# Performance work log

Hardware: AMD Instinct MI355X
Metric: run time of the kernel (lower is better)

## Reference

```python
import jax, jax.numpy as jnp
import numpy as np

B, S, F = 4, 2048, 8
D, H, L, FF = 256, 8, 2, 1024
DH = D // H
NSK, NPAT = 2000, 64
DQ = D // 4  # pattern/feat sub-embedding width


def setup_inputs() -> dict:
    key = jax.random.key(0)
    ks = jax.random.split(key, 32)
    r = lambda i, shape: jax.random.normal(ks[i], shape, jnp.float32) * 0.02
    return {
        'interactions': jax.random.randint(ks[0], (B, S), 0, 2 * NSK),
        'patterns': jax.random.randint(ks[1], (B, S), 0, NPAT),
        'forget_features': jax.random.normal(ks[2], (B, S, F), jnp.float32),
        'inter_emb': r(3, (2 * NSK, D)),
        'pattern_emb': r(4, (NPAT, DQ)),
        'feat_W': r(5, (F, DQ)), 'feat_b': jnp.zeros((DQ,), jnp.float32),
        'in_W': r(6, (D + 2 * DQ, D)), 'in_b': jnp.zeros((D,), jnp.float32),
        'time_W': r(7, (1, D)), 'time_b': jnp.zeros((D,), jnp.float32),
        'pos_W': r(8, (1, D)), 'pos_b': jnp.zeros((D,), jnp.float32),
        'Wq': r(9, (L, D, H, DH)), 'bq': jnp.zeros((L, H, DH), jnp.float32),
        'Wk': r(10, (L, D, H, DH)), 'bk': jnp.zeros((L, H, DH), jnp.float32),
        'Wv': r(11, (L, D, H, DH)), 'bv': jnp.zeros((L, H, DH), jnp.float32),
        'Wo': r(12, (L, H, DH, D)), 'bo': jnp.zeros((L, D), jnp.float32),
        'kerple_p': jnp.full((L, H, 1, 1), 0.5, jnp.float32),
        'kerple_a': jnp.zeros((L, H, 1, 1), jnp.float32),
        'ln1_g': jnp.ones((L, D), jnp.float32), 'ln1_b': jnp.zeros((L, D), jnp.float32),
        'ln2_g': jnp.ones((L, D), jnp.float32), 'ln2_b': jnp.zeros((L, D), jnp.float32),
        'ffn_W1': r(13, (L, D, FF)), 'ffn_b1': jnp.zeros((L, FF), jnp.float32),
        'ffn_W2': r(14, (L, FF, D)), 'ffn_b2': jnp.zeros((L, D), jnp.float32),
        'out_W': r(15, (D, NSK)), 'out_b': jnp.zeros((NSK,), jnp.float32),
    }


def _ln(x, g, b, eps=1e-6):
    m = jnp.mean(x, -1, keepdims=True)
    v = jnp.mean(jnp.square(x - m), -1, keepdims=True)
    return g * (x - m) * jax.lax.rsqrt(v + eps) + b


def reference(interactions, patterns, forget_features, inter_emb, pattern_emb,
              feat_W, feat_b, in_W, in_b, time_W, time_b, pos_W, pos_b,
              Wq, bq, Wk, bk, Wv, bv, Wo, bo, kerple_p, kerple_a,
              ln1_g, ln1_b, ln2_g, ln2_b, ffn_W1, ffn_b1, ffn_W2, ffn_b2,
              out_W, out_b):
    inter_e = inter_emb[interactions]                      # [B,S,D]
    pat_e = pattern_emb[patterns]                          # [B,S,D/4]
    feat_e = forget_features @ feat_W + feat_b             # [B,S,D/4]
    x = jnp.concatenate([inter_e, pat_e, feat_e], -1) @ in_W + in_b  # [B,S,D]
    elapsed = forget_features[:, :, 0:1]
    time_enc = jnp.tanh(elapsed @ time_W + time_b)
    pos = jnp.arange(S, dtype=jnp.float32)[None, :, None] / jnp.float32(S)
    pos_enc = pos @ pos_W + pos_b
    x = x + time_enc + pos_enc

    positions = jnp.arange(S, dtype=jnp.float32)
    dist = jnp.maximum(positions[:, None] - positions[None, :], 0.0)  # [S,S]
    causal_bias = jnp.triu(jnp.full((S, S), -1e9, jnp.float32), 1)    # [S,S]
    inv_sqrt_dh = 1.0 / jnp.sqrt(jnp.float32(DH))

    for i in range(L):
        p = jax.nn.softplus(kerple_p[i])                   # [H,1,1]
        a = jax.nn.softplus(kerple_a[i])
        bias = causal_bias[None] - p * jnp.log1p(a * dist[None])  # [H,S,S]
        q = jnp.einsum('bsd,dhk->bshk', x, Wq[i]) + bq[i]
        k = jnp.einsum('bsd,dhk->bshk', x, Wk[i]) + bk[i]
        v = jnp.einsum('bsd,dhk->bshk', x, Wv[i]) + bv[i]
        scores = jnp.einsum('bshk,bthk->bhst', q, k) * inv_sqrt_dh + bias[None]
        attn = jax.nn.softmax(scores, axis=-1)
        o = jnp.einsum('bhst,bthk->bshk', attn, v)
        attn_out = jnp.einsum('bshk,hkd->bsd', o, Wo[i]) + bo[i]
        x = _ln(x + attn_out, ln1_g[i], ln1_b[i])
        h = jax.nn.gelu(x @ ffn_W1[i] + ffn_b1[i], approximate=False)
        ffn_out = h @ ffn_W2[i] + ffn_b2[i]
        x = _ln(x + ffn_out, ln2_g[i], ln2_b[i])
    return x @ out_W + out_b
```

## Files before the change

kernel.cpp:

```cpp
#include <hip/hip_runtime.h>
#include <math.h>

#define SEQ   2048
#define BATCH 4
#define NTOK  8192
#define DM    256
#define NHD   8
#define DHD   32
#define DFF   1024
#define NSKC  2000

typedef __attribute__((ext_vector_type(8))) short short8;
typedef __attribute__((ext_vector_type(4))) float f32x4;
typedef unsigned short ushort_t;

#define QPRE ((float)(0.17677669529663687 * 1.4426950408889634))

#define SPERM(i) (((i) & ~31) | (((i) & 15) << 1) | (((i) >> 4) & 1))

__device__ __forceinline__ ushort_t f2bf(float x) {
    union { float f; unsigned u; } c; c.f = x;
    unsigned r = c.u + 0x7FFFu + ((c.u >> 16) & 1u);
    return (ushort_t)(r >> 16);
}

#if __has_builtin(__builtin_amdgcn_cvt_pk_bf16_f32)
typedef __attribute__((ext_vector_type(2))) __bf16 bf16x2_t;
__device__ __forceinline__ unsigned pack_bf16(float a, float b) {
    bf16x2_t r = __builtin_amdgcn_cvt_pk_bf16_f32(a, b);
    union { bf16x2_t v; unsigned u; } c; c.v = r;
    return c.u;
}
#else
__device__ __forceinline__ unsigned pack_bf16(float a, float b) {
    return (unsigned)f2bf(a) | ((unsigned)f2bf(b) << 16);
}
#endif

__device__ __forceinline__ float bf2f(ushort_t x) {
    union { unsigned u; float f; } c; c.u = ((unsigned)x) << 16;
    return c.f;
}

struct ConvSeg { const float* src; ushort_t* dst; int K; int N; int ntx; int base; int kperm; };
struct ConvArgs { ConvSeg s[14]; };

__global__ __launch_bounds__(256) void convert_kernel(ConvArgs args) {
    int bid = blockIdx.x;
    int si = 0;
#pragma unroll
    for (int i = 1; i < 14; i++) if (bid >= args.s[i].base) si = i;
    ConvSeg sg = args.s[si];
    int local = bid - sg.base;
    int ty = local / sg.ntx;
    int tx = local - ty * sg.ntx;
    int n0 = tx * 32, k0 = ty * 32;
    __shared__ float T[32][33];
    int tid = threadIdx.x;
    int tn = tid & 31, tk4 = tid >> 5;
#pragma unroll
    for (int i = 0; i < 4; i++) {
        int kl = tk4 + i * 8;
        float v = 0.0f;
        if (n0 + tn < sg.N) v = sg.src[(size_t)(k0 + kl) * sg.N + n0 + tn];
        T[kl][tn] = v;
    }
    __syncthreads();
    int tk = tid & 31, tn4 = tid >> 5;
    int tks = sg.kperm ? (((tk & 15) << 1) | ((tk >> 4) & 1)) : tk;
#pragma unroll
    for (int i = 0; i < 4; i++) {
        int nl = tn4 + i * 8;
        sg.dst[(size_t)(n0 + nl) * sg.K + k0 + tks] = f2bf(T[tk][nl]);
    }
}

__global__ __launch_bounds__(384) void concat_kernel(
    const int* __restrict__ interactions, const int* __restrict__ patterns,
    const float* __restrict__ ff, const float* __restrict__ inter_emb,
    const float* __restrict__ pattern_emb, const float* __restrict__ feat_W,
    const float* __restrict__ feat_b, ushort_t* __restrict__ out)
{
    int tok = blockIdx.x;
    int j = threadIdx.x;
    float v;
    if (j < 256) {
        v = inter_emb[(size_t)interactions[tok] * 256 + j];
    } else if (j < 320) {
        v = pattern_emb[patterns[tok] * 64 + (j - 256)];
    } else {
        int c = j - 320;
        float acc = feat_b[c];
#pragma unroll
        for (int f = 0; f < 8; f++) acc += ff[tok * 8 + f] * feat_W[f * 64 + c];
        v = acc;
    }
    out[(size_t)tok * 384 + j] = f2bf(v);
}

__global__ __launch_bounds__(256) void ln_kernel(
    float* __restrict__ x, const ushort_t* __restrict__ r,
    const float* __restrict__ g, const float* __restrict__ b,
    ushort_t* __restrict__ xb)
{
    int tok = blockIdx.x;
    int d = threadIdx.x;
    int ds = SPERM(d);
    size_t row = (size_t)tok * DM;
    float v = x[row + d] + bf2f(r[row + ds]);
    float s1 = v, s2 = v * v;
#pragma unroll
    for (int off = 32; off > 0; off >>= 1) {
        s1 += __shfl_down(s1, off, 64);
        s2 += __shfl_down(s2, off, 64);
    }
    __shared__ float red1[4], red2[4];
    int wid = d >> 6, lane = d & 63;
    if (lane == 0) { red1[wid] = s1; red2[wid] = s2; }
    __syncthreads();
    s1 = red1[0] + red1[1] + red1[2] + red1[3];
    s2 = red2[0] + red2[1] + red2[2] + red2[3];
    float mean = s1 * (1.0f / 256.0f);
    float var = s2 * (1.0f / 256.0f) - mean * mean;
    float inv = rsqrtf(var + 1e-6f);
    float nv = g[d] * (v - mean) * inv + b[d];
    x[row + d] = nv;
    xb[row + ds] = f2bf(nv);
}

__global__ __launch_bounds__(256) void gemm64(
    const ushort_t* __restrict__ A, const ushort_t* __restrict__ Bt,
    int M, int N, int K, int mode,
    float* __restrict__ Cf, ushort_t* __restrict__ Cb,
    const float* __restrict__ b0,
    const float* __restrict__ ffg, const float* __restrict__ tW,
    const float* __restrict__ tb, const float* __restrict__ pW,
    const float* __restrict__ pb)
{
    __shared__ ushort_t As[2][64][40];
    __shared__ ushort_t Bs[2][64][40];
    int m0 = blockIdx.x * 64, n0 = blockIdx.y * 64;
    int tid = threadIdx.x;
    int wv = tid >> 6, lane = tid & 63;
    int quad = lane >> 4, l16 = lane & 15;
    int srow = tid >> 2, sc = (tid & 3) << 3;

    f32x4 acc[4];
#pragma unroll
    for (int j = 0; j < 4; j++) acc[j] = (f32x4){0.f, 0.f, 0.f, 0.f};

    uint4 pa = *(const uint4*)&A[(size_t)(m0 + srow) * K + sc];
    uint4 pbv = *(const uint4*)&Bt[(size_t)(n0 + srow) * K + sc];
    *(uint4*)&As[0][srow][sc] = pa;
    *(uint4*)&Bs[0][srow][sc] = pbv;

    int mrow = wv * 16;
    for (int k0 = 0; k0 < K; k0 += 32) {
        int cur = (k0 >> 5) & 1;
        __syncthreads();
        bool more = (k0 + 32 < K);
        if (more) {
            pa = *(const uint4*)&A[(size_t)(m0 + srow) * K + k0 + 32 + sc];
            pbv = *(const uint4*)&Bt[(size_t)(n0 + srow) * K + k0 + 32 + sc];
        }
        short8 af = *(const short8*)&As[cur][mrow + l16][quad * 8];
        short8 bf0 = *(const short8*)&Bs[cur][l16][quad * 8];
        short8 bf1 = *(const short8*)&Bs[cur][16 + l16][quad * 8];
        short8 bf2 = *(const short8*)&Bs[cur][32 + l16][quad * 8];
        short8 bf3 = *(const short8*)&Bs[cur][48 + l16][quad * 8];
        acc[0] = __builtin_amdgcn_mfma_f32_16x16x32_bf16(af, bf0, acc[0], 0, 0, 0);
        acc[1] = __builtin_amdgcn_mfma_f32_16x16x32_bf16(af, bf1, acc[1], 0, 0, 0);
        acc[2] = __builtin_amdgcn_mfma_f32_16x16x32_bf16(af, bf2, acc[2], 0, 0, 0);
        acc[3] = __builtin_amdgcn_mfma_f32_16x16x32_bf16(af, bf3, acc[3], 0, 0, 0);
        if (more) {
            *(uint4*)&As[cur ^ 1][srow][sc] = pa;
            *(uint4*)&Bs[cur ^ 1][srow][sc] = pbv;
        }
    }

#pragma unroll
    for (int r = 0; r < 4; r++) {
        int m = m0 + mrow + quad * 4 + r;
        if (mode == 4) {
            int s = m & (SEQ - 1);
            float el = ffg[m * 8];
            float pos = (float)s * (1.0f / (float)SEQ);
#pragma unroll
            for (int nt = 0; nt < 4; nt += 2) {
                int nlo = n0 + nt * 16 + l16;
                int nhi = nlo + 16;
                float v0 = acc[nt][r] + b0[nlo] + tanhf(el * tW[nlo] + tb[nlo]) + pos * pW[nlo] + pb[nlo];
                float v1 = acc[nt + 1][r] + b0[nhi] + tanhf(el * tW[nhi] + tb[nhi]) + pos * pW[nhi] + pb[nhi];
                Cf[(size_t)m * N + nlo] = v0;
                Cf[(size_t)m * N + nhi] = v1;
                *(unsigned*)&Cb[(size_t)m * N + n0 + nt * 16 + 2 * l16] = pack_bf16(v0, v1);
            }
        } else {
#pragma unroll
            for (int nt = 0; nt < 4; nt += 2) {
                int nlo = n0 + nt * 16 + l16;
                float v0 = acc[nt][r] + b0[nlo];
                float v1 = acc[nt + 1][r] + b0[nlo + 16];
                *(unsigned*)&Cb[(size_t)m * N + n0 + nt * 16 + 2 * l16] = pack_bf16(v0, v1);
            }
        }
    }
}

__global__ __launch_bounds__(256) void gemm_db(
    const ushort_t* __restrict__ A, const ushort_t* __restrict__ Bt,
    int M, int N, int K, int mode,
    ushort_t* __restrict__ Cb, ushort_t* __restrict__ Ck, ushort_t* __restrict__ Cv,
    const float* __restrict__ b0, const float* __restrict__ b1,
    const float* __restrict__ b2)
{
    __shared__ ushort_t As[2][128][40];
    __shared__ ushort_t Bs[2][64][40];
    int m0 = blockIdx.x * 128, n0 = blockIdx.y * 64;
    int tid = threadIdx.x;
    int wv = tid >> 6, lane = tid & 63;
    int quad = lane >> 4, l16 = lane & 15;
    int srow = tid >> 2, sc = (tid & 3) << 3;

    f32x4 acc[2][4];
#pragma unroll
    for (int i = 0; i < 2; i++)
#pragma unroll
        for (int j = 0; j < 4; j++) acc[i][j] = (f32x4){0.f, 0.f, 0.f, 0.f};

    uint4 pa0 = *(const uint4*)&A[(size_t)(m0 + srow) * K + sc];
    uint4 pa1 = *(const uint4*)&A[(size_t)(m0 + 64 + srow) * K + sc];
    uint4 pbb = *(const uint4*)&Bt[(size_t)(n0 + srow) * K + sc];
    *(uint4*)&As[0][srow][sc] = pa0;
    *(uint4*)&As[0][64 + srow][sc] = pa1;
    *(uint4*)&Bs[0][srow][sc] = pbb;

    int msub = wv * 32;
    for (int k0 = 0; k0 < K; k0 += 32) {
        int cur = (k0 >> 5) & 1;
        __syncthreads();
        bool more = (k0 + 32 < K);
        if (more) {
            pa0 = *(const uint4*)&A[(size_t)(m0 + srow) * K + k0 + 32 + sc];
            pa1 = *(const uint4*)&A[(size_t)(m0 + 64 + srow) * K + k0 + 32 + sc];
            pbb = *(const uint4*)&Bt[(size_t)(n0 + srow) * K + k0 + 32 + sc];
        }
        short8 af0 = *(const short8*)&As[cur][msub + l16][quad * 8];
        short8 af1 = *(const short8*)&As[cur][msub + 16 + l16][quad * 8];
        short8 bf0 = *(const short8*)&Bs[cur][l16][quad * 8];
        short8 bf1 = *(const short8*)&Bs[cur][16 + l16][quad * 8];
        short8 bf2 = *(const short8*)&Bs[cur][32 + l16][quad * 8];
        short8 bf3 = *(const short8*)&Bs[cur][48 + l16][quad * 8];
        acc[0][0] = __builtin_amdgcn_mfma_f32_16x16x32_bf16(af0, bf0, acc[0][0], 0, 0, 0);
        acc[0][1] = __builtin_amdgcn_mfma_f32_16x16x32_bf16(af0, bf1, acc[0][1], 0, 0, 0);
        acc[0][2] = __builtin_amdgcn_mfma_f32_16x16x32_bf16(af0, bf2, acc[0][2], 0, 0, 0);
        acc[0][3] = __builtin_amdgcn_mfma_f32_16x16x32_bf16(af0, bf3, acc[0][3], 0, 0, 0);
        acc[1][0] = __builtin_amdgcn_mfma_f32_16x16x32_bf16(af1, bf0, acc[1][0], 0, 0, 0);
        acc[1][1] = __builtin_amdgcn_mfma_f32_16x16x32_bf16(af1, bf1, acc[1][1], 0, 0, 0);
        acc[1][2] = __builtin_amdgcn_mfma_f32_16x16x32_bf16(af1, bf2, acc[1][2], 0, 0, 0);
        acc[1][3] = __builtin_amdgcn_mfma_f32_16x16x32_bf16(af1, bf3, acc[1][3], 0, 0, 0);
        if (more) {
            *(uint4*)&As[cur ^ 1][srow][sc] = pa0;
            *(uint4*)&As[cur ^ 1][64 + srow][sc] = pa1;
            *(uint4*)&Bs[cur ^ 1][srow][sc] = pbb;
        }
    }

#pragma unroll
    for (int mt = 0; mt < 2; mt++) {
#pragma unroll
        for (int nt = 0; nt < 4; nt += 2) {
            int nlo = n0 + nt * 16 + l16;
#pragma unroll
            for (int r = 0; r < 4; r++) {
                int m = m0 + msub + mt * 16 + quad * 4 + r;
                float vlo = acc[mt][nt][r];
                float vhi = acc[mt][nt + 1][r];
                if (mode == 1) {
                    float t0 = vlo + b0[nlo];
                    float t1 = vhi + b0[nlo + 16];
                    t0 = 0.5f * t0 * (1.0f + erff(t0 * 0.70710678118654752f));
                    t1 = 0.5f * t1 * (1.0f + erff(t1 * 0.70710678118654752f));
                    *(unsigned*)&Cb[(size_t)m * N + n0 + nt * 16 + 2 * l16] = pack_bf16(t0, t1);
                } else {
                    int which = nlo >> 8, idx = nlo & 255;
                    int hh = idx >> 5;
                    int s = m & (SEQ - 1), b = m >> 11;
                    if (which == 0) {
                        float q0 = (vlo + b0[idx]) * QPRE;
                        float q1 = (vhi + b0[idx + 16]) * QPRE;
                        *(unsigned*)&Cb[(((size_t)(b * NHD + hh)) * SEQ + s) * DHD + 2 * l16] = pack_bf16(q0, q1);
                    } else if (which == 1) {
                        float k0v = vlo + b1[idx];
                        float k1v = vhi + b1[idx + 16];
                        *(unsigned*)&Ck[(((size_t)(b * NHD + hh)) * SEQ + s) * DHD + 2 * l16] = pack_bf16(k0v, k1v);
                    } else {
                        int sp = (s & ~31) | (((s & 15) << 1) | ((s >> 4) & 1));
                        Cv[(((size_t)(b * NHD + hh)) * DHD + l16) * SEQ + sp] = f2bf(vlo + b2[idx]);
                        Cv[(((size_t)(b * NHD + hh)) * DHD + l16 + 16) * SEQ + sp] = f2bf(vhi + b2[idx + 16]);
                    }
                }
            }
        }
    }
}

__global__ __launch_bounds__(256) void gemm_out(
    const ushort_t* __restrict__ A, const ushort_t* __restrict__ Bt,
    int M, int N, int K,
    float* __restrict__ Cf, const float* __restrict__ b0, int Nreal)
{
    __shared__ ushort_t As[2][128][40];
    __shared__ ushort_t Bs[2][128][40];
    int m0 = blockIdx.x * 128, n0 = blockIdx.y * 128;
    int tid = threadIdx.x;
    int wv = tid >> 6, lane = tid & 63;
    int quad = lane >> 4, l16 = lane & 15;
    int wm = (wv >> 1) * 64, wn = (wv & 1) * 64;
    int srow = tid >> 1, sc = (tid & 1) << 4;

    f32x4 acc[4][4];
#pragma unroll
    for (int i = 0; i < 4; i++)
#pragma unroll
        for (int j = 0; j < 4; j++) acc[i][j] = (f32x4){0.f, 0.f, 0.f, 0.f};

    uint4 pa0 = *(const uint4*)&A[(size_t)(m0 + srow) * K + sc];
    uint4 pa1 = *(const uint4*)&A[(size_t)(m0 + srow) * K + sc + 8];
    uint4 pb0 = *(const uint4*)&Bt[(size_t)(n0 + srow) * K + sc];
    uint4 pb1 = *(const uint4*)&Bt[(size_t)(n0 + srow) * K + sc + 8];
    *(uint4*)&As[0][srow][sc] = pa0;
    *(uint4*)&As[0][srow][sc + 8] = pa1;
    *(uint4*)&Bs[0][srow][sc] = pb0;
    *(uint4*)&Bs[0][srow][sc + 8] = pb1;

    for (int k0 = 0; k0 < K; k0 += 32) {
        int cur = (k0 >> 5) & 1;
        __syncthreads();
        bool more = (k0 + 32 < K);
        if (more) {
            pa0 = *(const uint4*)&A[(size_t)(m0 + srow) * K + k0 + 32 + sc];
            pa1 = *(const uint4*)&A[(size_t)(m0 + srow) * K + k0 + 32 + sc + 8];
            pb0 = *(const uint4*)&Bt[(size_t)(n0 + srow) * K + k0 + 32 + sc];
            pb1 = *(const uint4*)&Bt[(size_t)(n0 + srow) * K + k0 + 32 + sc + 8];
        }
        short8 af[4], bf[4];
#pragma unroll
        for (int i = 0; i < 4; i++) {
            af[i] = *(const short8*)&As[cur][wm + i * 16 + l16][quad * 8];
            bf[i] = *(const short8*)&Bs[cur][wn + i * 16 + l16][quad * 8];
        }
#pragma unroll
        for (int i = 0; i < 4; i++)
#pragma unroll
            for (int j = 0; j < 4; j++)
                acc[i][j] = __builtin_amdgcn_mfma_f32_16x16x32_bf16(af[i], bf[j], acc[i][j], 0, 0, 0);
        if (more) {
            *(uint4*)&As[cur ^ 1][srow][sc] = pa0;
            *(uint4*)&As[cur ^ 1][srow][sc + 8] = pa1;
            *(uint4*)&Bs[cur ^ 1][srow][sc] = pb0;
            *(uint4*)&Bs[cur ^ 1][srow][sc + 8] = pb1;
        }
    }

#pragma unroll
    for (int i = 0; i < 4; i++) {
#pragma unroll
        for (int j = 0; j < 4; j++) {
            int n = n0 + wn + j * 16 + l16;
            if (n < Nreal) {
#pragma unroll
                for (int r = 0; r < 4; r++) {
                    int m = m0 + wm + i * 16 + quad * 4 + r;
                    Cf[(size_t)m * Nreal + n] = acc[i][j][r] + b0[n];
                }
            }
        }
    }
}

__global__ __launch_bounds__(256) void attn_mfma(
    const ushort_t* __restrict__ qb, const ushort_t* __restrict__ kb,
    const ushort_t* __restrict__ vtb, const float* __restrict__ kp,
    const float* __restrict__ ka, ushort_t* __restrict__ ob)
{
    int h = blockIdx.y, b = blockIdx.z;
    int tid = threadIdx.x, wv = tid >> 6, lane = tid & 63;
    int quad = lane >> 4, l16 = lane & 15;

    __shared__ float tabs[2112];
    __shared__ __align__(16) float Cmbf[2][64][28];
    ushort_t* P2 = (ushort_t*)&Cmbf[0][0][0];

    float p = log1pf(__expf(kp[h]));
    float a = log1pf(__expf(ka[h]));
    for (int i = tid; i < 2112; i += 256) {
        float w = 0.0f;
        if (i >= 64) w = exp2f(-p * __log2f(fmaf(a, (float)(i - 64), 1.0f)));
        tabs[i] = w;
    }
    __syncthreads();

    int bh = b * NHD + h;
    const ushort_t* Qh = qb + (size_t)bh * SEQ * DHD;
    const ushort_t* Kh = kb + (size_t)bh * SEQ * DHD;
    const ushort_t* Vh = vtb + (size_t)bh * DHD * SEQ;

    int pj = blockIdx.x;
    int tlo = pj, thi = 127 - pj;
    int qlo0 = tlo * 16, qhi0 = thi * 16;

    short8 qfl = *(const short8*)&Qh[(qlo0 + l16) * DHD + quad * 8];
    short8 qfh = *(const short8*)&Qh[(qhi0 + l16) * DHD + quad * 8];
    f32x4 ol0 = (f32x4){0.f,0.f,0.f,0.f}, ol1 = (f32x4){0.f,0.f,0.f,0.f};
    f32x4 oh0 = (f32x4){0.f,0.f,0.f,0.f}, oh1 = (f32x4){0.f,0.f,0.f,0.f};
    float lsl[4] = {0.f,0.f,0.f,0.f}, lsh[4] = {0.f,0.f,0.f,0.f};
    ushort_t* Pl = P2 + wv * 1280;
    ushort_t* Ph = Pl + 640;

    int nch_hi = (thi + 2) >> 1;
    int nch_lo = (tlo + 2) >> 1;
    int qsrh = qhi0 + quad * 4;
    int qsrl = qlo0 + quad * 4;

    int ch = wv;
    short8 kf0n, kf1n;
    {
        int k0 = ch * 32;
        kf0n = *(const short8*)&Kh[(k0 + l16) * DHD + quad * 8];
        kf1n = *(const short8*)&Kh[(k0 + 16 + l16) * DHD + quad * 8];
    }

    for (; ch < nch_hi; ch += 4) {
        int k0 = ch * 32;
        short8 kf0 = kf0n, kf1 = kf1n;
        short8 vf0 = *(const short8*)&Vh[l16 * SEQ + k0 + quad * 8];
        short8 vf1 = *(const short8*)&Vh[(16 + l16) * SEQ + k0 + quad * 8];
        int chn = ch + 4;
        if (chn < nch_hi) {
            int kn = chn * 32;
            kf0n = *(const short8*)&Kh[(kn + l16) * DHD + quad * 8];
            kf1n = *(const short8*)&Kh[(kn + 16 + l16) * DHD + quad * 8];
        }
        f32x4 z = (f32x4){0.f,0.f,0.f,0.f};

        f32x4 s0 = __builtin_amdgcn_mfma_f32_16x16x32_bf16(qfh, kf0, z, 0, 0, 0);
        f32x4 s1 = __builtin_amdgcn_mfma_f32_16x16x32_bf16(qfh, kf1, z, 0, 0, 0);
        {
            const float* tp = &tabs[qsrh - k0 - l16 + 48];
#pragma unroll
            for (int r = 0; r < 4; r++) {
                float e0 = exp2f(s0[r]) * tp[16 + r];
                float e1 = exp2f(s1[r]) * tp[r];
                lsh[r] += e0 + e1;
                *(unsigned*)&Ph[(quad * 4 + r) * 40 + l16 * 2] = pack_bf16(e0, e1);
            }
        }
        bool do_lo = (ch < nch_lo);
        if (do_lo) {
            f32x4 t0 = __builtin_amdgcn_mfma_f32_16x16x32_bf16(qfl, kf0, z, 0, 0, 0);
            f32x4 t1 = __builtin_amdgcn_mfma_f32_16x16x32_bf16(qfl, kf1, z, 0, 0, 0);
            const float* tq = &tabs[qsrl - k0 - l16 + 48];
#pragma unroll
            for (int r = 0; r < 4; r++) {
                float e0 = exp2f(t0[r]) * tq[16 + r];
                float e1 = exp2f(t1[r]) * tq[r];
                lsl[r] += e0 + e1;
                *(unsigned*)&Pl[(quad * 4 + r) * 40 + l16 * 2] = pack_bf16(e0, e1);
            }
        }

        __builtin_amdgcn_wave_barrier();
        short8 pfh = *(const short8*)&Ph[l16 * 40 + quad * 8];
        oh0 = __builtin_amdgcn_mfma_f32_16x16x32_bf16(pfh, vf0, oh0, 0, 0, 0);
        oh1 = __builtin_amdgcn_mfma_f32_16x16x32_bf16(pfh, vf1, oh1, 0, 0, 0);
        if (do_lo) {
            short8 pfl = *(const short8*)&Pl[l16 * 40 + quad * 8];
            ol0 = __builtin_amdgcn_mfma_f32_16x16x32_bf16(pfl, vf0, ol0, 0, 0, 0);
            ol1 = __builtin_amdgcn_mfma_f32_16x16x32_bf16(pfl, vf1, ol1, 0, 0, 0);
        }
    }

    __syncthreads();
    float* cp = &Cmbf[wv >> 1][lane][0];
    if (wv & 1) {
        *(float4*)&cp[0]  = (float4){oh0[0], oh0[1], oh0[2], oh0[3]};
        *(float4*)&cp[4]  = (float4){oh1[0], oh1[1], oh1[2], oh1[3]};
        *(float4*)&cp[8]  = (float4){ol0[0], ol0[1], ol0[2], ol0[3]};
        *(float4*)&cp[12] = (float4){ol1[0], ol1[1], ol1[2], ol1[3]};
        *(float4*)&cp[16] = (float4){lsh[0], lsh[1], lsh[2], lsh[3]};
        *(float4*)&cp[20] = (float4){lsl[0], lsl[1], lsl[2], lsl[3]};
    }
    __syncthreads();
    if (!(wv & 1)) {
#pragma unroll
        for (int i = 0; i < 4; i++) {
            oh0[i] += cp[i];      oh1[i] += cp[4 + i];
            ol0[i] += cp[8 + i];  ol1[i] += cp[12 + i];
            lsh[i] += cp[16 + i]; lsl[i] += cp[20 + i];
        }
    }
    __syncthreads();
    if (wv == 2) {
        float* c0 = &Cmbf[0][lane][0];
        *(float4*)&c0[0]  = (float4){oh0[0], oh0[1], oh0[2], oh0[3]};
        *(float4*)&c0[4]  = (float4){oh1[0], oh1[1], oh1[2], oh1[3]};
        *(float4*)&c0[8]  = (float4){ol0[0], ol0[1], ol0[2], ol0[3]};
        *(float4*)&c0[12] = (float4){ol1[0], ol1[1], ol1[2], ol1[3]};
        *(float4*)&c0[16] = (float4){lsh[0], lsh[1], lsh[2], lsh[3]};
        *(float4*)&c0[20] = (float4){lsl[0], lsl[1], lsl[2], lsl[3]};
    }
    __syncthreads();
    if (wv == 0) {
        const float* c0 = &Cmbf[0][lane][0];
#pragma unroll
        for (int i = 0; i < 4; i++) {
            oh0[i] += c0[i];      oh1[i] += c0[4 + i];
            ol0[i] += c0[8 + i];  ol1[i] += c0[12 + i];
            lsh[i] += c0[16 + i]; lsl[i] += c0[20 + i];
        }
#pragma unroll
        for (int r = 0; r < 4; r++) {
#pragma unroll
            for (int off = 1; off < 16; off <<= 1) {
                lsh[r] += __shfl_xor(lsh[r], off, 16);
                lsl[r] += __shfl_xor(lsl[r], off, 16);
            }
        }
#pragma unroll
        for (int r = 0; r < 4; r++) {
            float rh = 1.0f / lsh[r];
            float rl = 1.0f / lsl[r];
            size_t bh_ = ((size_t)(b * SEQ + qsrh + r)) * DM + h * DHD;
            size_t bl_ = ((size_t)(b * SEQ + qsrl + r)) * DM + h * DHD;
            *(unsigned*)&ob[bh_ + 2 * l16] = pack_bf16(oh0[r] * rh, oh1[r] * rh);
            *(unsigned*)&ob[bl_ + 2 * l16] = pack_bf16(ol0[r] * rl, ol1[r] * rl);
        }
    }
}

extern "C" void kernel_launch(void* const* d_in, const int* in_sizes, int n_in,
                              void* d_out, int out_size, void* d_ws, size_t ws_size,
                              hipStream_t stream) {
    const int*   interactions = (const int*)d_in[0];
    const int*   patterns     = (const int*)d_in[1];
    const float* ff           = (const float*)d_in[2];
    const float* inter_emb    = (const float*)d_in[3];
    const float* pattern_emb  = (const float*)d_in[4];
    const float* feat_W       = (const float*)d_in[5];
    const float* feat_b       = (const float*)d_in[6];
    const float* in_W         = (const float*)d_in[7];
    const float* in_b         = (const float*)d_in[8];
    const float* time_W       = (const float*)d_in[9];
    const float* time_b       = (const float*)d_in[10];
    const float* pos_W        = (const float*)d_in[11];
    const float* pos_b        = (const float*)d_in[12];
    const float* Wq           = (const float*)d_in[13];
    const float* bq           = (const float*)d_in[14];
    const float* Wk           = (const float*)d_in[15];
    const float* bk           = (const float*)d_in[16];
    const float* Wv           = (const float*)d_in[17];
    const float* bv           = (const float*)d_in[18];
    const float* Wo           = (const float*)d_in[19];
    const float* bo           = (const float*)d_in[20];
    const float* kerple_p     = (const float*)d_in[21];
    const float* kerple_a     = (const float*)d_in[22];
    const float* ln1_g        = (const float*)d_in[23];
    const float* ln1_b        = (const float*)d_in[24];
    const float* ln2_g        = (const float*)d_in[25];
    const float* ln2_b        = (const float*)d_in[26];
    const float* ffn_W1       = (const float*)d_in[27];
    const float* ffn_b1       = (const float*)d_in[28];
    const float* ffn_W2       = (const float*)d_in[29];
    const float* ffn_b2       = (const float*)d_in[30];
    const float* out_W        = (const float*)d_in[31];
    const float* out_b        = (const float*)d_in[32];
    float* out = (float*)d_out;

    char* wsb = (char*)d_ws;
    const size_t MB = 1024 * 1024;
    float*    x    = (float*)(wsb + 0);
    ushort_t* tmpb = (ushort_t*)(wsb + 8  * MB);
    ushort_t* xb   = (ushort_t*)(wsb + 16 * MB);
    ushort_t* qbuf = (ushort_t*)(wsb + 20 * MB);
    ushort_t* kbuf = (ushort_t*)(wsb + 24 * MB);
    ushort_t* vtbf = (ushort_t*)(wsb + 28 * MB);
    ushort_t* shrd = (ushort_t*)(wsb + 32 * MB);
    ushort_t* cbuf = shrd;
    ushort_t* o_bf = shrd;
    ushort_t* h_bf = shrd;
    char* wp = wsb + 48 * MB;
    ushort_t* inWt  = (ushort_t*)wp;  wp += 256  * 384 * 2;
    ushort_t* qkvWt = (ushort_t*)wp;  wp += 2 * 768 * 256 * 2;
    ushort_t* WoT   = (ushort_t*)wp;  wp += 2 * 256 * 256 * 2;
    ushort_t* W1T   = (ushort_t*)wp;  wp += 2 * 1024 * 256 * 2;
    ushort_t* W2T   = (ushort_t*)wp;  wp += 2 * 256 * 1024 * 2;
    ushort_t* outWt = (ushort_t*)wp;  wp += 2048 * 256 * 2;

    ConvArgs ca;
    int D2 = 256 * 256;
    int base = 0, ib = 0;
    auto addseg = [&](const float* src, ushort_t* dst, int K, int N, int Npad, int kp) {
        ca.s[ib].src = src; ca.s[ib].dst = dst; ca.s[ib].K = K; ca.s[ib].N = N;
        ca.s[ib].ntx = Npad / 32; ca.s[ib].base = base; ca.s[ib].kperm = kp;
        base += (Npad / 32) * (K / 32); ib++;
    };
    addseg(in_W,            inWt,           384,  256,  256,  0);
    addseg(Wq,              qkvWt,          256,  256,  256,  1);
    addseg(Wk,              qkvWt + 1 * D2, 256,  256,  256,  1);
    addseg(Wv,              qkvWt + 2 * D2, 256,  256,  256,  1);
    addseg(Wq + D2,         qkvWt + 3 * D2, 256,  256,  256,  1);
    addseg(Wk + D2,         qkvWt + 4 * D2, 256,  256,  256,  1);
    addseg(Wv + D2,         qkvWt + 5 * D2, 256,  256,  256,  1);
    addseg(Wo,              WoT,            256,  256,  256,  1);
    addseg(Wo + D2,         WoT + D2,       256,  256,  256,  1);
    addseg(ffn_W1,          W1T,            256,  1024, 1024, 1);
    addseg(ffn_W1 + 4 * D2, W1T + 4 * D2,   256,  1024, 1024, 1);
    addseg(ffn_W2,          W2T,            1024, 256,  256,  1);
    addseg(ffn_W2 + 4 * D2, W2T + 4 * D2,   1024, 256,  256,  1);
    addseg(out_W,           outWt,          256,  2000, 2048, 1);
    convert_kernel<<<base, 256, 0, stream>>>(ca);

    concat_kernel<<<NTOK, 384, 0, stream>>>(interactions, patterns, ff,
                                            inter_emb, pattern_emb, feat_W, feat_b, cbuf);
    gemm64<<<dim3(128, 4), 256, 0, stream>>>(cbuf, inWt, NTOK, 256, 384, 4,
                                             x, xb, in_b, ff, time_W, time_b, pos_W, pos_b);

    for (int l = 0; l < 2; l++) {
        gemm_db<<<dim3(64, 12), 256, 0, stream>>>(
            xb, qkvWt + (size_t)l * 768 * 256, NTOK, 768, 256, 2,
            qbuf, kbuf, vtbf, bq + l * 256, bk + l * 256, bv + l * 256);
        attn_mfma<<<dim3(64, NHD, BATCH), 256, 0, stream>>>(
            qbuf, kbuf, vtbf, kerple_p + l * NHD, kerple_a + l * NHD, o_bf);
        gemm64<<<dim3(128, 4), 256, 0, stream>>>(
            o_bf, WoT + (size_t)l * D2, NTOK, 256, 256, 5,
            nullptr, tmpb, bo + l * 256, nullptr, nullptr, nullptr, nullptr, nullptr);
        ln_kernel<<<NTOK, 256, 0, stream>>>(x, tmpb, ln1_g + l * 256, ln1_b + l * 256, xb);
        gemm_db<<<dim3(64, 16), 256, 0, stream>>>(
            xb, W1T + (size_t)l * 4 * D2, NTOK, 1024, 256, 1,
            h_bf, nullptr, nullptr, ffn_b1 + l * 1024, nullptr, nullptr);
        gemm64<<<dim3(128, 4), 256, 0, stream>>>(
            h_bf, W2T + (size_t)l * 4 * D2, NTOK, 256, 1024, 5,
            nullptr, tmpb, ffn_b2 + l * 256, nullptr, nullptr, nullptr, nullptr, nullptr);
        ln_kernel<<<NTOK, 256, 0, stream>>>(x, tmpb, ln2_g + l * 256, ln2_b + l * 256, xb);
    }

    gemm_out<<<dim3(64, 16), 256, 0, stream>>>(
        xb, outWt, NTOK, 2048, 256, out, out_b, NSKC);
}
```

Baseline: 416.2 us.

## Keep attention probabilities in registers by computing transposed scores with K-row permutation

After: 403.0 us. -3.2%, faster.

```diff
diff --git a/kernel.cpp b/kernel.cpp
--- a/kernel.cpp
+++ b/kernel.cpp
@@ -37,9 +37,21 @@
 }
 #endif
 
+#if __has_builtin(__builtin_amdgcn_exp2f)
+__device__ __forceinline__ float fexp2(float x) { return __builtin_amdgcn_exp2f(x); }
+#else
+__device__ __forceinline__ float fexp2(float x) { return exp2f(x); }
+#endif
+
 __device__ __forceinline__ float bf2f(ushort_t x) {
     union { unsigned u; float f; } c; c.u = ((unsigned)x) << 16;
     return c.f;
+}
+
+__device__ __forceinline__ short8 mk_s8(unsigned a, unsigned b, unsigned c, unsigned d) {
+    union { unsigned u[4]; short8 s; } t;
+    t.u[0] = a; t.u[1] = b; t.u[2] = c; t.u[3] = d;
+    return t.s;
 }
 
 struct ConvSeg { const float* src; ushort_t* dst; int K; int N; int ntx; int base; int kperm; };
@@ -295,9 +307,8 @@
                         float k1v = vhi + b1[idx + 16];
                         *(unsigned*)&Ck[(((size_t)(b * NHD + hh)) * SEQ + s) * DHD + 2 * l16] = pack_bf16(k0v, k1v);
                     } else {
-                        int sp = (s & ~31) | (((s & 15) << 1) | ((s >> 4) & 1));
-                        Cv[(((size_t)(b * NHD + hh)) * DHD + l16) * SEQ + sp] = f2bf(vlo + b2[idx]);
-                        Cv[(((size_t)(b * NHD + hh)) * DHD + l16 + 16) * SEQ + sp] = f2bf(vhi + b2[idx + 16]);
+                        Cv[(((size_t)(b * NHD + hh)) * DHD + l16) * SEQ + s] = f2bf(vlo + b2[idx]);
+                        Cv[(((size_t)(b * NHD + hh)) * DHD + l16 + 16) * SEQ + s] = f2bf(vhi + b2[idx + 16]);
                     }
                 }
             }
@@ -384,19 +395,23 @@
     const ushort_t* __restrict__ vtb, const float* __restrict__ kp,
     const float* __restrict__ ka, ushort_t* __restrict__ ob)
 {
-    int h = blockIdx.y, b = blockIdx.z;
+    int gid = blockIdx.x;
+    int hb = ((gid >> 9) << 3) | (gid & 7);
+    int pj = (gid >> 3) & 63;
+    int b = hb >> 3, h = hb & 7;
+
     int tid = threadIdx.x, wv = tid >> 6, lane = tid & 63;
     int quad = lane >> 4, l16 = lane & 15;
 
     __shared__ float tabs[2112];
-    __shared__ __align__(16) float Cmbf[2][64][28];
-    ushort_t* P2 = (ushort_t*)&Cmbf[0][0][0];
+    __shared__ __align__(16) float ShA[2560];
+    __shared__ float LsB[128];
 
     float p = log1pf(__expf(kp[h]));
     float a = log1pf(__expf(ka[h]));
     for (int i = tid; i < 2112; i += 256) {
         float w = 0.0f;
-        if (i >= 64) w = exp2f(-p * __log2f(fmaf(a, (float)(i - 64), 1.0f)));
+        if (i >= 64) w = fexp2(-p * __log2f(fmaf(a, (float)(i - 64), 1.0f)));
         tabs[i] = w;
     }
     __syncthreads();
@@ -406,7 +421,6 @@
     const ushort_t* Kh = kb + (size_t)bh * SEQ * DHD;
     const ushort_t* Vh = vtb + (size_t)bh * DHD * SEQ;
 
-    int pj = blockIdx.x;
     int tlo = pj, thi = 127 - pj;
     int qlo0 = tlo * 16, qhi0 = thi * 16;
 
@@ -414,21 +428,20 @@
     short8 qfh = *(const short8*)&Qh[(qhi0 + l16) * DHD + quad * 8];
     f32x4 ol0 = (f32x4){0.f,0.f,0.f,0.f}, ol1 = (f32x4){0.f,0.f,0.f,0.f};
     f32x4 oh0 = (f32x4){0.f,0.f,0.f,0.f}, oh1 = (f32x4){0.f,0.f,0.f,0.f};
-    float lsl[4] = {0.f,0.f,0.f,0.f}, lsh[4] = {0.f,0.f,0.f,0.f};
-    ushort_t* Pl = P2 + wv * 1280;
-    ushort_t* Ph = Pl + 640;
+    float lsh_s = 0.f, lsl_s = 0.f;
 
     int nch_hi = (thi + 2) >> 1;
     int nch_lo = (tlo + 2) >> 1;
-    int qsrh = qhi0 + quad * 4;
-    int qsrl = qlo0 + quad * 4;
+    int krow = ((l16 >> 2) << 3) | (l16 & 3);
+    int tb_h = qhi0 + l16 + 64 - 8 * quad;
+    int tb_l = qlo0 + l16 + 64 - 8 * quad;
 
     int ch = wv;
     short8 kf0n, kf1n;
     {
         int k0 = ch * 32;
-        kf0n = *(const short8*)&Kh[(k0 + l16) * DHD + quad * 8];
-        kf1n = *(const short8*)&Kh[(k0 + 16 + l16) * DHD + quad * 8];
+        kf0n = *(const short8*)&Kh[(k0 + krow) * DHD + quad * 8];
+        kf1n = *(const short8*)&Kh[(k0 + 4 + krow) * DHD + quad * 8];
     }
 
     for (; ch < nch_hi; ch += 4) {
@@ -439,57 +452,70 @@
         int chn = ch + 4;
         if (chn < nch_hi) {
             int kn = chn * 32;
-            kf0n = *(const short8*)&Kh[(kn + l16) * DHD + quad * 8];
-            kf1n = *(const short8*)&Kh[(kn + 16 + l16) * DHD + quad * 8];
+            kf0n = *(const short8*)&Kh[(kn + krow) * DHD + quad * 8];
+            kf1n = *(const short8*)&Kh[(kn + 4 + krow) * DHD + quad * 8];
         }
         f32x4 z = (f32x4){0.f,0.f,0.f,0.f};
 
-        f32x4 s0 = __builtin_amdgcn_mfma_f32_16x16x32_bf16(qfh, kf0, z, 0, 0, 0);
-        f32x4 s1 = __builtin_amdgcn_mfma_f32_16x16x32_bf16(qfh, kf1, z, 0, 0, 0);
+        f32x4 s0 = __builtin_amdgcn_mfma_f32_16x16x32_bf16(kf0, qfh, z, 0, 0, 0);
+        f32x4 s1 = __builtin_amdgcn_mfma_f32_16x16x32_bf16(kf1, qfh, z, 0, 0, 0);
         {
-            const float* tp = &tabs[qsrh - k0 - l16 + 48];
-#pragma unroll
-            for (int r = 0; r < 4; r++) {
-                float e0 = exp2f(s0[r]) * tp[16 + r];
-                float e1 = exp2f(s1[r]) * tp[r];
-                lsh[r] += e0 + e1;
-                *(unsigned*)&Ph[(quad * 4 + r) * 40 + l16 * 2] = pack_bf16(e0, e1);
-            }
-        }
-        bool do_lo = (ch < nch_lo);
-        if (do_lo) {
-            f32x4 t0 = __builtin_amdgcn_mfma_f32_16x16x32_bf16(qfl, kf0, z, 0, 0, 0);
-            f32x4 t1 = __builtin_amdgcn_mfma_f32_16x16x32_bf16(qfl, kf1, z, 0, 0, 0);
-            const float* tq = &tabs[qsrl - k0 - l16 + 48];
-#pragma unroll
-            for (int r = 0; r < 4; r++) {
-                float e0 = exp2f(t0[r]) * tq[16 + r];
-                float e1 = exp2f(t1[r]) * tq[r];
-                lsl[r] += e0 + e1;
-                *(unsigned*)&Pl[(quad * 4 + r) * 40 + l16 * 2] = pack_bf16(e0, e1);
-            }
-        }
-
-        __builtin_amdgcn_wave_barrier();
-        short8 pfh = *(const short8*)&Ph[l16 * 40 + quad * 8];
-        oh0 = __builtin_amdgcn_mfma_f32_16x16x32_bf16(pfh, vf0, oh0, 0, 0, 0);
-        oh1 = __builtin_amdgcn_mfma_f32_16x16x32_bf16(pfh, vf1, oh1, 0, 0, 0);
-        if (do_lo) {
-            short8 pfl = *(const short8*)&Pl[l16 * 40 + quad * 8];
-            ol0 = __builtin_amdgcn_mfma_f32_16x16x32_bf16(pfl, vf0, ol0, 0, 0, 0);
-            ol1 = __builtin_amdgcn_mfma_f32_16x16x32_bf16(pfl, vf1, ol1, 0, 0, 0);
-        }
-    }
-
-    __syncthreads();
-    float* cp = &Cmbf[wv >> 1][lane][0];
+            const float* tp = &tabs[tb_h - k0];
+            float e0 = fexp2(s0[0]) * tp[0];
+            float e1 = fexp2(s0[1]) * tp[-1];
+            float e2 = fexp2(s0[2]) * tp[-2];
+            float e3 = fexp2(s0[3]) * tp[-3];
+            unsigned p0 = pack_bf16(e0, e1);
+            unsigned p1 = pack_bf16(e2, e3);
+            float f0 = fexp2(s1[0]) * tp[-4];
+            float f1 = fexp2(s1[1]) * tp[-5];
+            float f2 = fexp2(s1[2]) * tp[-6];
+            float f3 = fexp2(s1[3]) * tp[-7];
+            unsigned p2 = pack_bf16(f0, f1);
+            unsigned p3 = pack_bf16(f2, f3);
+            lsh_s += ((e0 + e1) + (e2 + e3)) + ((f0 + f1) + (f2 + f3));
+            short8 pf = mk_s8(p0, p1, p2, p3);
+            oh0 = __builtin_amdgcn_mfma_f32_16x16x32_bf16(pf, vf0, oh0, 0, 0, 0);
+            oh1 = __builtin_amdgcn_mfma_f32_16x16x32_bf16(pf, vf1, oh1, 0, 0, 0);
+        }
+        if (ch < nch_lo) {
+            f32x4 t0 = __builtin_amdgcn_mfma_f32_16x16x32_bf16(kf0, qfl, z, 0, 0, 0);
+            f32x4 t1 = __builtin_amdgcn_mfma_f32_16x16x32_bf16(kf1, qfl, z, 0, 0, 0);
+            const float* tq = &tabs[tb_l - k0];
+            float e0 = fexp2(t0[0]) * tq[0];
+            float e1 = fexp2(t0[1]) * tq[-1];
+            float e2 = fexp2(t0[2]) * tq[-2];
+            float e3 = fexp2(t0[3]) * tq[-3];
+            unsigned p0 = pack_bf16(e0, e1);
+            unsigned p1 = pack_bf16(e2, e3);
+            float f0 = fexp2(t1[0]) * tq[-4];
+            float f1 = fexp2(t1[1]) * tq[-5];
+            float f2 = fexp2(t1[2]) * tq[-6];
+            float f3 = fexp2(t1[3]) * tq[-7];
+            unsigned p2 = pack_bf16(f0, f1);
+            unsigned p3 = pack_bf16(f2, f3);
+            lsl_s += ((e0 + e1) + (e2 + e3)) + ((f0 + f1) + (f2 + f3));
+            short8 pf = mk_s8(p0, p1, p2, p3);
+            ol0 = __builtin_amdgcn_mfma_f32_16x16x32_bf16(pf, vf0, ol0, 0, 0, 0);
+            ol1 = __builtin_amdgcn_mfma_f32_16x16x32_bf16(pf, vf1, ol1, 0, 0, 0);
+        }
+    }
+
+    lsh_s += __shfl_xor(lsh_s, 16, 64);
+    lsh_s += __shfl_xor(lsh_s, 32, 64);
+    lsl_s += __shfl_xor(lsl_s, 16, 64);
+    lsl_s += __shfl_xor(lsl_s, 32, 64);
+    if (lane < 16) {
+        LsB[wv * 32 + lane] = lsh_s;
+        LsB[wv * 32 + 16 + lane] = lsl_s;
+    }
+
+    float* cp = &ShA[((wv >> 1) * 64 + lane) * 20];
     if (wv & 1) {
         *(float4*)&cp[0]  = (float4){oh0[0], oh0[1], oh0[2], oh0[3]};
         *(float4*)&cp[4]  = (float4){oh1[0], oh1[1], oh1[2], oh1[3]};
         *(float4*)&cp[8]  = (float4){ol0[0], ol0[1], ol0[2], ol0[3]};
         *(float4*)&cp[12] = (float4){ol1[0], ol1[1], ol1[2], ol1[3]};
-        *(float4*)&cp[16] = (float4){lsh[0], lsh[1], lsh[2], lsh[3]};
-        *(float4*)&cp[20] = (float4){lsl[0], lsl[1], lsl[2], lsl[3]};
     }
     __syncthreads();
     if (!(wv & 1)) {
@@ -497,40 +523,32 @@
         for (int i = 0; i < 4; i++) {
             oh0[i] += cp[i];      oh1[i] += cp[4 + i];
             ol0[i] += cp[8 + i];  ol1[i] += cp[12 + i];
-            lsh[i] += cp[16 + i]; lsl[i] += cp[20 + i];
         }
     }
     __syncthreads();
     if (wv == 2) {
-        float* c0 = &Cmbf[0][lane][0];
+        float* c0 = &ShA[lane * 20];
         *(float4*)&c0[0]  = (float4){oh0[0], oh0[1], oh0[2], oh0[3]};
         *(float4*)&c0[4]  = (float4){oh1[0], oh1[1], oh1[2], oh1[3]};
         *(float4*)&c0[8]  = (float4){ol0[0], ol0[1], ol0[2], ol0[3]};
         *(float4*)&c0[12] = (float4){ol1[0], ol1[1], ol1[2], ol1[3]};
-        *(float4*)&c0[16] = (float4){lsh[0], lsh[1], lsh[2], lsh[3]};
-        *(float4*)&c0[20] = (float4){lsl[0], lsl[1], lsl[2], lsl[3]};
     }
     __syncthreads();
     if (wv == 0) {
-        const float* c0 = &Cmbf[0][lane][0];
+        const float* c0 = &ShA[lane * 20];
 #pragma unroll
         for (int i = 0; i < 4; i++) {
             oh0[i] += c0[i];      oh1[i] += c0[4 + i];
             ol0[i] += c0[8 + i];  ol1[i] += c0[12 + i];
-            lsh[i] += c0[16 + i]; lsl[i] += c0[20 + i];
-        }
+        }
+        int qr = quad * 4;
+        int qsrh = qhi0 + qr, qsrl = qlo0 + qr;
 #pragma unroll
         for (int r = 0; r < 4; r++) {
-#pragma unroll
-            for (int off = 1; off < 16; off <<= 1) {
-                lsh[r] += __shfl_xor(lsh[r], off, 16);
-                lsl[r] += __shfl_xor(lsl[r], off, 16);
-            }
-        }
-#pragma unroll
-        for (int r = 0; r < 4; r++) {
-            float rh = 1.0f / lsh[r];
-            float rl = 1.0f / lsl[r];
+            float dh = (LsB[qr + r] + LsB[32 + qr + r]) + (LsB[64 + qr + r] + LsB[96 + qr + r]);
+            float dl = (LsB[16 + qr + r] + LsB[48 + qr + r]) + (LsB[80 + qr + r] + LsB[112 + qr + r]);
+            float rh = 1.0f / dh;
+            float rl = 1.0f / dl;
             size_t bh_ = ((size_t)(b * SEQ + qsrh + r)) * DM + h * DHD;
             size_t bl_ = ((size_t)(b * SEQ + qsrl + r)) * DM + h * DHD;
             *(unsigned*)&ob[bh_ + 2 * l16] = pack_bf16(oh0[r] * rh, oh1[r] * rh);
@@ -630,7 +648,7 @@
         gemm_db<<<dim3(64, 12), 256, 0, stream>>>(
             xb, qkvWt + (size_t)l * 768 * 256, NTOK, 768, 256, 2,
             qbuf, kbuf, vtbf, bq + l * 256, bk + l * 256, bv + l * 256);
-        attn_mfma<<<dim3(64, NHD, BATCH), 256, 0, stream>>>(
+        attn_mfma<<<2048, 256, 0, stream>>>(
             qbuf, kbuf, vtbf, kerple_p + l * NHD, kerple_a + l * NHD, o_bf);
         gemm64<<<dim3(128, 4), 256, 0, stream>>>(
             o_bf, WoT + (size_t)l * D2, NTOK, 256, 256, 5,
```
